# Optimization experiments

Measured on AMD Instinct MI355X. Metric: run time of the kernel, lower is better.

## Reference

```python
import jax, jax.numpy as jnp
import numpy as np

NUM_USERS = 100000
NUM_ITEMS = 50000
EMBED_DIM = 64
NUM_LAYERS = 3
NUM_EDGES = 1250000
N = NUM_USERS + NUM_ITEMS


def setup_inputs() -> dict:
    key = jax.random.key(0)
    k1, k2, k3 = jax.random.split(key, 3)
    edge_index = jax.random.randint(k1, (2, NUM_EDGES), 0, N, dtype=jnp.int64)
    # nn.init.normal_(std=0.1)
    user_weight = 0.1 * jax.random.normal(k2, (NUM_USERS, EMBED_DIM), dtype=jnp.float32)
    item_weight = 0.1 * jax.random.normal(k3, (NUM_ITEMS, EMBED_DIM), dtype=jnp.float32)
    return {"edge_index": edge_index, "user_weight": user_weight, "item_weight": item_weight}


def reference(edge_index, user_weight, item_weight):
    src = edge_index[0]  # [E]
    dst = edge_index[1]  # [E]
    # degrees counted from dst column only (matches the torch loop)
    deg = jax.ops.segment_sum(jnp.ones_like(src, dtype=jnp.float32), dst, num_segments=N)
    norm = 1.0 / (jnp.sqrt(deg[src]) * jnp.sqrt(deg[dst]))  # [E]
    norm = jnp.where(jnp.isfinite(norm), norm, 0.0)

    emb = jnp.concatenate([user_weight, item_weight], axis=0)  # [N, D]
    acc = emb  # running sum over layer outputs (incl. layer 0)
    cur = emb
    for _ in range(NUM_LAYERS):
        msgs = cur[src] * norm[:, None]  # [E, D]
        cur = jax.ops.segment_sum(msgs, dst, num_segments=N)
        acc = acc + cur
    all_embeddings = acc / (NUM_LAYERS + 1)
    user_embeddings = all_embeddings[:NUM_USERS]
    item_embeddings = all_embeddings[NUM_USERS:]
    return all_embeddings, user_embeddings, item_embeddings
```

## Files before the change

### kernel.cpp

```cpp
#include <hip/hip_runtime.h>


#define NU 100000
#define NI 50000
#define NN 150000
#define DIM 64
#define NE 1250000
#define NF (NN * DIM)
#define NF4 (NF / 4)
#define SLOT 40
#define NBK 293
#define BSTRIDE 5120
#define PB 256
#define EPB ((NE + PB - 1) / PB)

typedef unsigned short ushort_t;

__device__ inline ushort_t f2bf(float f) {
    unsigned u = __float_as_uint(f);
    return (ushort_t)((u + 0x7FFF + ((u >> 16) & 1)) >> 16);
}
__device__ inline float bflo(unsigned u) { return __uint_as_float(u << 16); }
__device__ inline float bfhi(unsigned u) { return __uint_as_float(u & 0xffff0000u); }

__global__ void __launch_bounds__(1024) phaseA_kernel(const int* __restrict__ src,
                                                      const int* __restrict__ dst,
                                                      int* __restrict__ bcursor,
                                                      int2* __restrict__ part) {
    __shared__ int hist[NBK];
    __shared__ int cur[NBK];
    int b = blockIdx.x;
    int tid = threadIdx.x;
    if (tid < NBK) hist[tid] = 0;
    __syncthreads();
    int e0 = b * EPB;
    int e1 = min(e0 + EPB, NE);
    for (int e = e0 + tid; e < e1; e += 1024)
        atomicAdd(&hist[dst[e] >> 9], 1);
    __syncthreads();
    if (tid < NBK) {
        int h = hist[tid];
        int base = h ? atomicAdd(&bcursor[tid], h) : 0;
        cur[tid] = tid * BSTRIDE + base;
    }
    __syncthreads();
    for (int e = e0 + tid; e < e1; e += 1024) {
        int d = dst[e];
        int s = src[e];
        int p = atomicAdd(&cur[d >> 9], 1);
        part[p] = make_int2(s, d);
    }
}

__global__ void __launch_bounds__(1024) phaseB_kernel(const int* __restrict__ bcursor,
                                                      const int2* __restrict__ part,
                                                      int* __restrict__ cursor,
                                                      float* __restrict__ rdeg,
                                                      int* __restrict__ slots,
                                                      const float4* __restrict__ uw4,
                                                      const float4* __restrict__ iw4,
                                                      ushort_t* __restrict__ embb) {
    __shared__ int dcount[512];
    __shared__ float rfs[512];
    int b = blockIdx.x;
    int tid = threadIdx.x;
    int cnt = min(bcursor[b], BSTRIDE);
    int nodebase = b * 512;
    if (tid < 512) dcount[tid] = 0;
    __syncthreads();
    const int2* pb = part + b * BSTRIDE;
    for (int i = tid; i < cnt; i += 1024) {
        int2 e = pb[i];
        int dloc = e.y - nodebase;
        int p = atomicAdd(&dcount[dloc], 1);
        slots[(nodebase + dloc) * SLOT + p] = e.x;
    }
    __syncthreads();
    if (tid < 512) {
        int n = nodebase + tid;
        float r = 0.0f;
        if (n < NN) {
            int c = dcount[tid];
            cursor[n] = c;
            r = (c > 0) ? rsqrtf((float)c) : 0.0f;
            rdeg[n] = r;
        }
        rfs[tid] = r;
    }
    __syncthreads();
    int nnode = min(512, NN - nodebase);
    int lim = nnode * 16;
    for (int q = tid; q < lim; q += 1024) {
        int nl = q >> 4;
        int node = nodebase + nl;
        int c4 = q & 15;
        float4 v = (node < NU) ? uw4[node * 16 + c4] : iw4[(node - NU) * 16 + c4];
        float r = rfs[nl];
        ushort4 h;
        h.x = f2bf(v.x * r); h.y = f2bf(v.y * r);
        h.z = f2bf(v.z * r); h.w = f2bf(v.w * r);
        *(ushort4*)(embb + node * DIM + c4 * 4) = h;
    }
}

template <int LAYER>
__global__ void __launch_bounds__(256) gather_kernel(const int* __restrict__ cursor,
                                                     const float* __restrict__ rdeg,
                                                     const int* __restrict__ slots,
                                                     const ushort_t* __restrict__ cur,
                                                     const float4* __restrict__ uw4,
                                                     const float4* __restrict__ iw4,
                                                     float4* __restrict__ acc,
                                                     ushort_t* __restrict__ nxt) {
    int n = blockIdx.x * 4 + (threadIdx.x >> 6);
    int lane = threadIdx.x & 63;
    int j = lane >> 4;
    int d = lane & 15;
    bool j1 = (j & 1) != 0;
    bool j2 = (j & 2) != 0;
    int dg = __builtin_amdgcn_readfirstlane(cursor[n]);
    float rd = __uint_as_float(__builtin_amdgcn_readfirstlane(__float_as_uint(rdeg[n])));
    const int* sb = slots + __builtin_amdgcn_readfirstlane(n) * SLOT;
    float a0 = 0.0f, a1 = 0.0f, a2 = 0.0f, a3 = 0.0f;

    for (int c = 0; c < dg; c += 8) {
        int4 qa = *(const int4*)(sb + c);
        int4 qb = *(const int4*)(sb + c + 4);
        int ta = j1 ? qa.y : qa.x;
        int tb = j1 ? qa.w : qa.z;
        int sva = j2 ? tb : ta;
        int tc = j1 ? qb.y : qb.x;
        int td = j1 ? qb.w : qb.z;
        int svb = j2 ? td : tc;
        bool va = (c + j) < dg;
        bool vb = (c + 4 + j) < dg;
        sva = va ? sva : 0;
        svb = vb ? svb : 0;
        uint2 ua = *((const uint2*)(cur + sva * DIM) + d);
        uint2 ub = *((const uint2*)(cur + svb * DIM) + d);
        float wa = va ? 1.0f : 0.0f;
        float wb = vb ? 1.0f : 0.0f;
        a0 = fmaf(wa, bflo(ua.x), a0); a1 = fmaf(wa, bfhi(ua.x), a1);
        a2 = fmaf(wa, bflo(ua.y), a2); a3 = fmaf(wa, bfhi(ua.y), a3);
        a0 = fmaf(wb, bflo(ub.x), a0); a1 = fmaf(wb, bfhi(ub.x), a1);
        a2 = fmaf(wb, bflo(ub.y), a2); a3 = fmaf(wb, bfhi(ub.y), a3);
    }

    a0 += __shfl_xor(a0, 16); a1 += __shfl_xor(a1, 16);
    a2 += __shfl_xor(a2, 16); a3 += __shfl_xor(a3, 16);
    a0 += __shfl_xor(a0, 32); a1 += __shfl_xor(a1, 32);
    a2 += __shfl_xor(a2, 32); a3 += __shfl_xor(a3, 32);

    float c0 = rd * a0, c1 = rd * a1, c2 = rd * a2, c3 = rd * a3;
    int idx4 = n * 16 + d;

    if (j == 0) {
        if (LAYER == 1) {
            float4 e = (n < NU) ? uw4[n * 16 + d] : iw4[(n - NU) * 16 + d];
            acc[idx4] = make_float4(e.x + c0, e.y + c1, e.z + c2, e.w + c3);
            ushort4 h;
            h.x = f2bf(rd * c0); h.y = f2bf(rd * c1);
            h.z = f2bf(rd * c2); h.w = f2bf(rd * c3);
            *(ushort4*)(nxt + n * DIM + d * 4) = h;
        } else if (LAYER == 2) {
            float4 t = acc[idx4];
            acc[idx4] = make_float4(t.x + c0, t.y + c1, t.z + c2, t.w + c3);
            ushort4 h;
            h.x = f2bf(rd * c0); h.y = f2bf(rd * c1);
            h.z = f2bf(rd * c2); h.w = f2bf(rd * c3);
            *(ushort4*)(nxt + n * DIM + d * 4) = h;
        } else {
            float4 t = acc[idx4];
            float4 v = make_float4((t.x + c0) * 0.25f, (t.y + c1) * 0.25f,
                                   (t.z + c2) * 0.25f, (t.w + c3) * 0.25f);
            acc[idx4] = v;
            acc[NF4 + idx4] = v;
        }
    }
}

extern "C" void kernel_launch(void* const* d_in, const int* in_sizes, int n_in,
                              void* d_out, int out_size, void* d_ws, size_t ws_size,
                              hipStream_t stream) {
    const int* edge = (const int*)d_in[0];
    const int* src = edge;
    const int* dst = edge + NE;
    const float* uw = (const float*)d_in[1];
    const float* iw = (const float*)d_in[2];
    float* out = (float*)d_out;

    int* cursor    = (int*)d_ws;
    float* rdeg    = (float*)(cursor + NN);
    int* bcursor   = (int*)(rdeg + NN);
    int* slots     = bcursor + 320;
    int2* part     = (int2*)(slots + NN * SLOT);
    ushort_t* embb = (ushort_t*)(part + NBK * BSTRIDE);
    ushort_t* bufA = embb;
    ushort_t* bufT = (ushort_t*)(out + NF);

    hipMemsetAsync(bcursor, 0, NBK * sizeof(int), stream);
    phaseA_kernel<<<PB, 1024, 0, stream>>>(src, dst, bcursor, part);
    phaseB_kernel<<<NBK, 1024, 0, stream>>>(bcursor, part, cursor, rdeg, slots,
                                            (const float4*)uw, (const float4*)iw, embb);

    gather_kernel<1><<<NN / 4, 256, 0, stream>>>(cursor, rdeg, slots, embb,
                                                 (const float4*)uw, (const float4*)iw,
                                                 (float4*)out, bufT);
    gather_kernel<2><<<NN / 4, 256, 0, stream>>>(cursor, rdeg, slots, bufT,
                                                 (const float4*)uw, (const float4*)iw,
                                                 (float4*)out, bufA);
    gather_kernel<3><<<NN / 4, 256, 0, stream>>>(cursor, rdeg, slots, bufA,
                                                 (const float4*)uw, (const float4*)iw,
                                                 (float4*)out, nullptr);
}
```

Before: 303.0 us.

## Pack partition entries, pad slots with zero sentinel, gather two nodes per wave

Partition entries are packed into a single int (local dst in the high bits, src in the low 18 bits), which halves the scatter and read traffic between the two setup phases. Slot lists are padded up to a multiple of 8 with a sentinel index that points at a zeroed row, so the gather loop can drop its validity predicates and weight multiplies. Each wave now handles two nodes, n and n+75000, with independent accumulators, giving more memory-level parallelism, and blocks grow to 1024 threads. The change also clamps degree at SLOT, which alters results for nodes with more neighbours than that, and it depends on the sentinel rows just past the bf16 buffers being zeroed.

```diff
diff --git a/kernel.cpp b/kernel.cpp
--- a/kernel.cpp
+++ b/kernel.cpp
@@ -4,6 +4,7 @@
 #define NU 100000
 #define NI 50000
 #define NN 150000
+#define HALF 75000
 #define DIM 64
 #define NE 1250000
 #define NF (NN * DIM)
@@ -26,7 +27,7 @@
 __global__ void __launch_bounds__(1024) phaseA_kernel(const int* __restrict__ src,
                                                       const int* __restrict__ dst,
                                                       int* __restrict__ bcursor,
-                                                      int2* __restrict__ part) {
+                                                      int* __restrict__ part) {
     __shared__ int hist[NBK];
     __shared__ int cur[NBK];
     int b = blockIdx.x;
@@ -45,15 +46,15 @@
     }
     __syncthreads();
     for (int e = e0 + tid; e < e1; e += 1024) {
-        int d = dst[e];
+        int dd = dst[e];
         int s = src[e];
-        int p = atomicAdd(&cur[d >> 9], 1);
-        part[p] = make_int2(s, d);
+        int p = atomicAdd(&cur[dd >> 9], 1);
+        part[p] = ((dd & 511) << 18) | s;
     }
 }
 
 __global__ void __launch_bounds__(1024) phaseB_kernel(const int* __restrict__ bcursor,
-                                                      const int2* __restrict__ part,
+                                                      const int* __restrict__ part,
                                                       int* __restrict__ cursor,
                                                       float* __restrict__ rdeg,
                                                       int* __restrict__ slots,
@@ -68,22 +69,26 @@
     int nodebase = b * 512;
     if (tid < 512) dcount[tid] = 0;
     __syncthreads();
-    const int2* pb = part + b * BSTRIDE;
+    const int* pb = part + b * BSTRIDE;
     for (int i = tid; i < cnt; i += 1024) {
-        int2 e = pb[i];
-        int dloc = e.y - nodebase;
+        int v = pb[i];
+        int dloc = v >> 18;
         int p = atomicAdd(&dcount[dloc], 1);
-        slots[(nodebase + dloc) * SLOT + p] = e.x;
+        if (p < SLOT)
+            slots[(nodebase + dloc) * SLOT + p] = v & 0x3FFFF;
     }
     __syncthreads();
     if (tid < 512) {
         int n = nodebase + tid;
         float r = 0.0f;
         if (n < NN) {
-            int c = dcount[tid];
+            int c = min(dcount[tid], SLOT);
             cursor[n] = c;
             r = (c > 0) ? rsqrtf((float)c) : 0.0f;
             rdeg[n] = r;
+            int e = (c <= 8) ? 8 : ((c + 7) & ~7);
+            for (int k = c; k < e; k++)
+                slots[n * SLOT + k] = NN;
         }
         rfs[tid] = r;
     }
@@ -104,77 +109,106 @@
 }
 
 template <int LAYER>
-__global__ void __launch_bounds__(256) gather_kernel(const int* __restrict__ cursor,
-                                                     const float* __restrict__ rdeg,
-                                                     const int* __restrict__ slots,
-                                                     const ushort_t* __restrict__ cur,
-                                                     const float4* __restrict__ uw4,
-                                                     const float4* __restrict__ iw4,
-                                                     float4* __restrict__ acc,
-                                                     ushort_t* __restrict__ nxt) {
-    int n = blockIdx.x * 4 + (threadIdx.x >> 6);
+__global__ void __launch_bounds__(1024) gather_kernel(const int* __restrict__ cursor,
+                                                      const float* __restrict__ rdeg,
+                                                      const int* __restrict__ slots,
+                                                      const ushort_t* __restrict__ cur,
+                                                      const float4* __restrict__ uw4,
+                                                      const float4* __restrict__ iw4,
+                                                      float4* __restrict__ acc,
+                                                      ushort_t* __restrict__ nxt) {
+    int wid = blockIdx.x * 16 + (threadIdx.x >> 6);
+    int n0 = __builtin_amdgcn_readfirstlane(wid);
+    if (n0 >= HALF) return;
+    int n1 = n0 + HALF;
     int lane = threadIdx.x & 63;
     int j = lane >> 4;
     int d = lane & 15;
     bool j1 = (j & 1) != 0;
     bool j2 = (j & 2) != 0;
-    int dg = __builtin_amdgcn_readfirstlane(cursor[n]);
-    float rd = __uint_as_float(__builtin_amdgcn_readfirstlane(__float_as_uint(rdeg[n])));
-    const int* sb = slots + __builtin_amdgcn_readfirstlane(n) * SLOT;
-    float a0 = 0.0f, a1 = 0.0f, a2 = 0.0f, a3 = 0.0f;
-
-    for (int c = 0; c < dg; c += 8) {
-        int4 qa = *(const int4*)(sb + c);
-        int4 qb = *(const int4*)(sb + c + 4);
-        int ta = j1 ? qa.y : qa.x;
-        int tb = j1 ? qa.w : qa.z;
-        int sva = j2 ? tb : ta;
-        int tc = j1 ? qb.y : qb.x;
-        int td = j1 ? qb.w : qb.z;
-        int svb = j2 ? td : tc;
-        bool va = (c + j) < dg;
-        bool vb = (c + 4 + j) < dg;
-        sva = va ? sva : 0;
-        svb = vb ? svb : 0;
-        uint2 ua = *((const uint2*)(cur + sva * DIM) + d);
-        uint2 ub = *((const uint2*)(cur + svb * DIM) + d);
-        float wa = va ? 1.0f : 0.0f;
-        float wb = vb ? 1.0f : 0.0f;
-        a0 = fmaf(wa, bflo(ua.x), a0); a1 = fmaf(wa, bfhi(ua.x), a1);
-        a2 = fmaf(wa, bflo(ua.y), a2); a3 = fmaf(wa, bfhi(ua.y), a3);
-        a0 = fmaf(wb, bflo(ub.x), a0); a1 = fmaf(wb, bfhi(ub.x), a1);
-        a2 = fmaf(wb, bflo(ub.y), a2); a3 = fmaf(wb, bfhi(ub.y), a3);
-    }
+    int dg0 = __builtin_amdgcn_readfirstlane(cursor[n0]);
+    int dg1 = __builtin_amdgcn_readfirstlane(cursor[n1]);
+    float rd0 = __uint_as_float(__builtin_amdgcn_readfirstlane(__float_as_uint(rdeg[n0])));
+    float rd1 = __uint_as_float(__builtin_amdgcn_readfirstlane(__float_as_uint(rdeg[n1])));
+    const int* sb0 = slots + n0 * SLOT;
+    const int* sb1 = slots + n1 * SLOT;
+    float a0 = 0, a1 = 0, a2 = 0, a3 = 0;
+    float b0 = 0, b1 = 0, b2 = 0, b3 = 0;
+
+#define GRP(SB, C, X0, X1, X2, X3)                                             \
+    {                                                                          \
+        int4 qa = *(const int4*)((SB) + (C));                                  \
+        int4 qb = *(const int4*)((SB) + (C) + 4);                              \
+        int ta = j1 ? qa.y : qa.x;                                             \
+        int tb = j1 ? qa.w : qa.z;                                             \
+        int sva = j2 ? tb : ta;                                                \
+        int tc = j1 ? qb.y : qb.x;                                             \
+        int td = j1 ? qb.w : qb.z;                                             \
+        int svb = j2 ? td : tc;                                                \
+        uint2 ua = *((const uint2*)(cur + sva * DIM) + d);                     \
+        uint2 ub = *((const uint2*)(cur + svb * DIM) + d);                     \
+        X0 += bflo(ua.x); X1 += bfhi(ua.x);                                    \
+        X2 += bflo(ua.y); X3 += bfhi(ua.y);                                    \
+        X0 += bflo(ub.x); X1 += bfhi(ub.x);                                    \
+        X2 += bflo(ub.y); X3 += bfhi(ub.y);                                    \
+    }
+
+    GRP(sb0, 0, a0, a1, a2, a3)
+    GRP(sb1, 0, b0, b1, b2, b3)
+    for (int c = 8; c < dg0; c += 8) GRP(sb0, c, a0, a1, a2, a3)
+    for (int c = 8; c < dg1; c += 8) GRP(sb1, c, b0, b1, b2, b3)
+#undef GRP
 
     a0 += __shfl_xor(a0, 16); a1 += __shfl_xor(a1, 16);
     a2 += __shfl_xor(a2, 16); a3 += __shfl_xor(a3, 16);
+    b0 += __shfl_xor(b0, 16); b1 += __shfl_xor(b1, 16);
+    b2 += __shfl_xor(b2, 16); b3 += __shfl_xor(b3, 16);
     a0 += __shfl_xor(a0, 32); a1 += __shfl_xor(a1, 32);
     a2 += __shfl_xor(a2, 32); a3 += __shfl_xor(a3, 32);
-
-    float c0 = rd * a0, c1 = rd * a1, c2 = rd * a2, c3 = rd * a3;
-    int idx4 = n * 16 + d;
+    b0 += __shfl_xor(b0, 32); b1 += __shfl_xor(b1, 32);
+    b2 += __shfl_xor(b2, 32); b3 += __shfl_xor(b3, 32);
+
+    float c00 = rd0 * a0, c01 = rd0 * a1, c02 = rd0 * a2, c03 = rd0 * a3;
+    float c10 = rd1 * b0, c11 = rd1 * b1, c12 = rd1 * b2, c13 = rd1 * b3;
 
     if (j == 0) {
+        int i0 = n0 * 16 + d;
+        int i1 = n1 * 16 + d;
         if (LAYER == 1) {
-            float4 e = (n < NU) ? uw4[n * 16 + d] : iw4[(n - NU) * 16 + d];
-            acc[idx4] = make_float4(e.x + c0, e.y + c1, e.z + c2, e.w + c3);
-            ushort4 h;
-            h.x = f2bf(rd * c0); h.y = f2bf(rd * c1);
-            h.z = f2bf(rd * c2); h.w = f2bf(rd * c3);
-            *(ushort4*)(nxt + n * DIM + d * 4) = h;
+            float4 e0 = uw4[n0 * 16 + d];
+            float4 e1 = (n1 < NU) ? uw4[n1 * 16 + d] : iw4[(n1 - NU) * 16 + d];
+            acc[i0] = make_float4(e0.x + c00, e0.y + c01, e0.z + c02, e0.w + c03);
+            acc[i1] = make_float4(e1.x + c10, e1.y + c11, e1.z + c12, e1.w + c13);
+            ushort4 h0, h1;
+            h0.x = f2bf(rd0 * c00); h0.y = f2bf(rd0 * c01);
+            h0.z = f2bf(rd0 * c02); h0.w = f2bf(rd0 * c03);
+            h1.x = f2bf(rd1 * c10); h1.y = f2bf(rd1 * c11);
+            h1.z = f2bf(rd1 * c12); h1.w = f2bf(rd1 * c13);
+            *(ushort4*)(nxt + n0 * DIM + d * 4) = h0;
+            *(ushort4*)(nxt + n1 * DIM + d * 4) = h1;
         } else if (LAYER == 2) {
-            float4 t = acc[idx4];
-            acc[idx4] = make_float4(t.x + c0, t.y + c1, t.z + c2, t.w + c3);
-            ushort4 h;
-            h.x = f2bf(rd * c0); h.y = f2bf(rd * c1);
-            h.z = f2bf(rd * c2); h.w = f2bf(rd * c3);
-            *(ushort4*)(nxt + n * DIM + d * 4) = h;
+            float4 t0 = acc[i0];
+            float4 t1 = acc[i1];
+            acc[i0] = make_float4(t0.x + c00, t0.y + c01, t0.z + c02, t0.w + c03);
+            acc[i1] = make_float4(t1.x + c10, t1.y + c11, t1.z + c12, t1.w + c13);
+            ushort4 h0, h1;
+            h0.x = f2bf(rd0 * c00); h0.y = f2bf(rd0 * c01);
+            h0.z = f2bf(rd0 * c02); h0.w = f2bf(rd0 * c03);
+            h1.x = f2bf(rd1 * c10); h1.y = f2bf(rd1 * c11);
+            h1.z = f2bf(rd1 * c12); h1.w = f2bf(rd1 * c13);
+            *(ushort4*)(nxt + n0 * DIM + d * 4) = h0;
+            *(ushort4*)(nxt + n1 * DIM + d * 4) = h1;
         } else {
-            float4 t = acc[idx4];
-            float4 v = make_float4((t.x + c0) * 0.25f, (t.y + c1) * 0.25f,
-                                   (t.z + c2) * 0.25f, (t.w + c3) * 0.25f);
-            acc[idx4] = v;
-            acc[NF4 + idx4] = v;
+            float4 t0 = acc[i0];
+            float4 t1 = acc[i1];
+            float4 v0 = make_float4((t0.x + c00) * 0.25f, (t0.y + c01) * 0.25f,
+                                    (t0.z + c02) * 0.25f, (t0.w + c03) * 0.25f);
+            float4 v1 = make_float4((t1.x + c10) * 0.25f, (t1.y + c11) * 0.25f,
+                                    (t1.z + c12) * 0.25f, (t1.w + c13) * 0.25f);
+            acc[i0] = v0;
+            acc[NF4 + i0] = v0;
+            acc[i1] = v1;
+            acc[NF4 + i1] = v1;
         }
     }
 }
@@ -193,23 +227,28 @@
     float* rdeg    = (float*)(cursor + NN);
     int* bcursor   = (int*)(rdeg + NN);
     int* slots     = bcursor + 320;
-    int2* part     = (int2*)(slots + NN * SLOT);
+    int* part      = slots + NN * SLOT;
     ushort_t* embb = (ushort_t*)(part + NBK * BSTRIDE);
     ushort_t* bufA = embb;
     ushort_t* bufT = (ushort_t*)(out + NF);
 
     hipMemsetAsync(bcursor, 0, NBK * sizeof(int), stream);
+    hipMemsetAsync(embb + NF, 0, DIM * sizeof(ushort_t), stream);
+    hipMemsetAsync(bufT + NF, 0, DIM * sizeof(ushort_t), stream);
+
     phaseA_kernel<<<PB, 1024, 0, stream>>>(src, dst, bcursor, part);
     phaseB_kernel<<<NBK, 1024, 0, stream>>>(bcursor, part, cursor, rdeg, slots,
                                             (const float4*)uw, (const float4*)iw, embb);
 
-    gather_kernel<1><<<NN / 4, 256, 0, stream>>>(cursor, rdeg, slots, embb,
-                                                 (const float4*)uw, (const float4*)iw,
-                                                 (float4*)out, bufT);
-    gather_kernel<2><<<NN / 4, 256, 0, stream>>>(cursor, rdeg, slots, bufT,
-                                                 (const float4*)uw, (const float4*)iw,
-                                                 (float4*)out, bufA);
-    gather_kernel<3><<<NN / 4, 256, 0, stream>>>(cursor, rdeg, slots, bufA,
-                                                 (const float4*)uw, (const float4*)iw,
-                                                 (float4*)out, nullptr);
-}
+    const int GB = (HALF + 15) / 16;
+
+    gather_kernel<1><<<GB, 1024, 0, stream>>>(cursor, rdeg, slots, embb,
+                                              (const float4*)uw, (const float4*)iw,
+                                              (float4*)out, bufT);
+    gather_kernel<2><<<GB, 1024, 0, stream>>>(cursor, rdeg, slots, bufT,
+                                              (const float4*)uw, (const float4*)iw,
+                                              (float4*)out, bufA);
+    gather_kernel<3><<<GB, 1024, 0, stream>>>(cursor, rdeg, slots, bufA,
+                                              (const float4*)uw, (const float4*)iw,
+                                              (float4*)out, nullptr);
+}
```

Measured after the change: 284.2 us. 6.2% less time.
